# Optimization experiments

Measured on AMD Instinct MI355X. Metric: run time of the kernel, lower is better.

## Reference

```python
import jax, jax.numpy as jnp
import numpy as np

WS = 7  # window_size (odd)


def _attn_idx(H, W, ws):
    # replication-pad the arange over the valid (unfolded) grid, matching ReplicationPad2d
    Ho, Wo = H - (ws - 1), W - (ws - 1)
    idx = np.arange(Ho * Wo, dtype=np.int64).reshape(Ho, Wo)
    pad = ws // 2
    idx = np.pad(idx, pad, mode='edge')  # [H, W]
    return jnp.asarray(idx.reshape(-1))  # [H*W]


def _bias_idx(H, W, ws):
    rep_h = np.ones(ws, dtype=np.int64); rep_h[ws // 2] = H - (ws - 1)
    rep_w = np.ones(ws, dtype=np.int64); rep_w[ws // 2] = W - (ws - 1)
    idx_h = np.repeat(np.arange(ws), rep_h)  # [H]
    idx_w = np.repeat(np.arange(ws), rep_w)  # [W]
    bias_hw = idx_h[:, None] * (2 * ws - 1) + idx_w[None, :]  # [H, W]
    idx_k = (np.arange(ws)[:, None] * (2 * ws - 1) + np.arange(ws)).reshape(-1)  # [ws^2]
    bias_idx = bias_hw.reshape(-1)[:, None] + idx_k[None, :]  # [H*W, ws^2]
    return jnp.asarray(bias_idx)


def setup_inputs() -> dict:
    key = jax.random.key(0)
    k0, k1, k2, k3 = jax.random.split(key, 4)
    B, C, H, W = 2, 256, 56, 56
    nh = 8
    x = jax.random.normal(k0, (B, C, H, W), jnp.float32)
    qkv_w = jax.random.normal(k1, (3 * C, C), jnp.float32) * 0.02  # 1x1 conv weight
    qkv_b = jnp.zeros((3 * C,), jnp.float32)
    proj_w = jax.random.normal(k2, (C, C), jnp.float32) * 0.02  # 1x1 conv weight
    proj_b = jnp.zeros((C,), jnp.float32)
    relative_bias = jax.random.normal(k3, ((2 * WS - 1) ** 2, nh), jnp.float32) * 0.02
    return {"x": x, "qkv_w": qkv_w, "qkv_b": qkv_b,
            "proj_w": proj_w, "proj_b": proj_b, "relative_bias": relative_bias}


def reference(x, qkv_w, qkv_b, proj_w, proj_b, relative_bias):
    B, C, H, W = x.shape
    ws = WS
    nh = relative_bias.shape[1]
    hd = C // nh
    scale = hd ** -0.5
    L = (H - ws + 1) * (W - ws + 1)

    # 1x1 conv qkv
    qkv = jnp.einsum('oc,bchw->bohw', qkv_w, x) + qkv_b[None, :, None, None]
    q, k, v = qkv[:, :C], qkv[:, C:2 * C], qkv[:, 2 * C:]
    q = q * scale

    def unfold(t):
        # torch nn.Unfold: [B, C*ws^2, L] with channel-major ordering (c slowest),
        # then .view(B, C, -1, ws^2): row-major reinterpretation (faithful to source)
        p = jax.lax.conv_general_dilated_patches(t, (ws, ws), (1, 1), 'VALID')  # [B,C*ws^2,Ho,Wo]
        return p.reshape(B, C, L, ws * ws)

    attn_idx = _attn_idx(H, W, ws)   # [H*W] indices into L
    bias_idx = _bias_idx(H, W, ws)   # [H*W, ws^2]

    k_u = unfold(k).reshape(B, nh, hd, L, ws * ws).transpose(0, 1, 3, 2, 4)  # [B,nh,L,hd,ws^2]
    v_u = unfold(v).reshape(B, nh, hd, L, ws * ws).transpose(0, 1, 3, 4, 2)  # [B,nh,L,ws^2,hd]
    k_g = k_u[:, :, attn_idx]  # [B,nh,HW,hd,ws^2]
    v_g = v_u[:, :, attn_idx]  # [B,nh,HW,ws^2,hd]

    qh = q.reshape(B, nh, hd, H * W).transpose(0, 1, 3, 2)  # [B,nh,HW,hd]

    attn = jnp.einsum('bnld,bnldk->bnlk', qh, k_g)  # [B,nh,HW,ws^2]
    bias = jnp.transpose(relative_bias[bias_idx], (2, 0, 1))  # [nh,HW,ws^2]
    attn = attn + bias[None]  # NOTE: source applies no softmax; dropout p=0

    out = jnp.einsum('bnlk,bnlkd->bnld', attn, v_g)  # [B,nh,HW,hd]
    out = jnp.transpose(out, (0, 1, 3, 2)).reshape(B, C, H, W)
    out = jnp.einsum('oc,bchw->bohw', proj_w, out) + proj_b[None, :, None, None]
    return out
```

## Files before the change

kernel.cpp:

```cpp
#include <hip/hip_runtime.h>
#include <cstddef>
#include <cstdint>

#define HWT   3136
#define WIMG  56
#define CCH   256
#define NH    8
#define QKV_ELEMS (16 * HWT * 32)
#define SCALE 0.17677669529663687f

typedef __attribute__((ext_vector_type(8))) short short8;
typedef __attribute__((ext_vector_type(4))) short short4v;
typedef __attribute__((ext_vector_type(4))) float f32x4;
typedef _Float16 half2v __attribute__((ext_vector_type(2)));
typedef _Float16 half4v __attribute__((ext_vector_type(4)));
typedef _Float16 half8v __attribute__((ext_vector_type(8)));

#if defined(__has_builtin)
#if __has_builtin(__builtin_amdgcn_fdot2)
#define HAVE_FDOT2 1
#endif
#endif
#ifndef HAVE_FDOT2
#define HAVE_FDOT2 0
#endif

__device__ __forceinline__ ushort f2bf(float f) {
  union { float f; uint32_t u; } v; v.f = f;
  uint32_t u = v.u;
  u += 0x7fffu + ((u >> 16) & 1u);
  return (ushort)(u >> 16);
}

__global__ __launch_bounds__(256) void prep_k(
    const float* __restrict__ x, const float* __restrict__ qkv_w,
    const float* __restrict__ proj_w, ushort* __restrict__ xt,
    ushort* __restrict__ wq, ushort* __restrict__ wp,
    ushort* __restrict__ src16) {
  if (blockIdx.z == 3) {
    int e = (blockIdx.y * 98 + blockIdx.x) * 256 + threadIdx.x;
    if (e < 2500 * 49) {
      int sp = e / 2500;
      int pos = e - sp * 2500;
      int i = pos / 50 + sp / 7;
      int j = pos % 50 + sp % 7;
      src16[e] = (ushort)(i * WIMG + j);
    }
    return;
  }
  if (blockIdx.z == 2) {
    int base = ((blockIdx.y * 98 + blockIdx.x) * 256 + threadIdx.x) * 2;
#pragma unroll
    for (int e = base; e < base + 2; ++e) {
      if (e < 768 * 256) wq[e] = f2bf(qkv_w[e]);
      else if (e < 768 * 256 + 256 * 256) {
        int e2 = e - 768 * 256;
        wp[e2] = f2bf(proj_w[e2]);
      }
    }
    return;
  }
  __shared__ float tile[32][33];
  const int hw0 = blockIdx.x * 32, c0 = blockIdx.y * 32, b = blockIdx.z;
  const int tx = threadIdx.x & 31, ty = threadIdx.x >> 5;
  const float* xb = x + ((size_t)b * CCH + c0) * HWT + hw0;
#pragma unroll
  for (int i = 0; i < 4; ++i) {
    int c = ty + i * 8;
    tile[c][tx] = xb[(size_t)c * HWT + tx];
  }
  __syncthreads();
  ushort* xo = xt + ((size_t)b * HWT + hw0) * CCH + c0;
#pragma unroll
  for (int i = 0; i < 4; ++i) {
    int hwl = ty + i * 8;
    xo[(size_t)hwl * CCH + tx] = f2bf(tile[tx][hwl]);
  }
}

template <int MODE, int MI>
__global__ __launch_bounds__(256) void mfma_gemm_k(
    const ushort* __restrict__ A, int rowsA,
    const ushort* __restrict__ B, int rowsB,
    const float* __restrict__ biasv, void* __restrict__ outp) {
  __shared__ ushort Alds[MI * 32 * 32];
  __shared__ ushort Blds[64 * 32];

  const int t  = threadIdx.x;
  const int m0 = blockIdx.y * (MI * 32);
  const int n0 = blockIdx.x * 64;
  const int b  = blockIdx.z;

  const ushort* Ab = A;
  const ushort* Bb = B + (size_t)b * HWT * CCH;

  const int lane  = t & 63;
  const int wid   = t >> 6;
  const int wm    = (wid >> 1) * (MI * 16);
  const int wn    = (wid & 1) * 32;
  const int lrow  = lane & 15;
  const int cwant = lane >> 4;
  const int csw   = (cwant ^ ((lrow >> 1) & 3)) * 8;

  const int srow   = t >> 2;
  const int scslot = t & 3;
  const int wlds   = wid << 9;

  f32x4 acc[MI][2];
#pragma unroll
  for (int i = 0; i < MI; ++i)
#pragma unroll
    for (int j = 0; j < 2; ++j) acc[i][j] = (f32x4){0.f, 0.f, 0.f, 0.f};

  for (int k0 = 0; k0 < CCH; k0 += 32) {
    __syncthreads();
#pragma unroll
    for (int h = 0; h < (MI + 1) / 2; ++h) {
      const int lr = srow + h * 64;
      if (lr < MI * 32) {
        const int csrc = (scslot ^ ((lr >> 1) & 3)) * 8;
        int ga = m0 + lr; ga = ga < rowsA ? ga : rowsA - 1;
        const ushort* gpa = Ab + (size_t)ga * CCH + k0 + csrc;
        ushort* lpa = Alds + h * 2048 + wlds;
        __builtin_amdgcn_global_load_lds(
            (const __attribute__((address_space(1))) void*)gpa,
            (__attribute__((address_space(3))) void*)lpa, 16, 0, 0);
      }
    }
    {
      const int lr = srow;
      const int csrc = (scslot ^ ((lr >> 1) & 3)) * 8;
      int gb = n0 + lr; gb = gb < rowsB ? gb : rowsB - 1;
      const ushort* gpb = Bb + (size_t)gb * CCH + k0 + csrc;
      ushort* lpb = Blds + wlds;
      __builtin_amdgcn_global_load_lds(
          (const __attribute__((address_space(1))) void*)gpb,
          (__attribute__((address_space(3))) void*)lpb, 16, 0, 0);
    }
    __syncthreads();

    short8 af[MI], bf[2];
#pragma unroll
    for (int mi = 0; mi < MI; ++mi)
      af[mi] = *(const short8*)&Alds[(wm + mi * 16 + lrow) * 32 + csw];
#pragma unroll
    for (int ni = 0; ni < 2; ++ni)
      bf[ni] = *(const short8*)&Blds[(wn + ni * 16 + lrow) * 32 + csw];
#pragma unroll
    for (int mi = 0; mi < MI; ++mi)
#pragma unroll
      for (int ni = 0; ni < 2; ++ni)
        acc[mi][ni] = __builtin_amdgcn_mfma_f32_16x16x32_bf16(
            af[mi], bf[ni], acc[mi][ni], 0, 0, 0);
  }

  const int row4 = (lane >> 4) * 4;
  if (MODE == 0) {
    _Float16* qh = (_Float16*)outp;
#pragma unroll
    for (int mi = 0; mi < MI; ++mi) {
      const int o0 = m0 + wm + mi * 16 + row4;
      const int t3 = o0 >> 8, c0 = o0 & 255;
      const int head = c0 >> 5, d0 = c0 & 31;
      const float sc = (t3 == 0) ? SCALE : 1.f;
      float bv[4];
#pragma unroll
      for (int r = 0; r < 4; ++r) bv[r] = biasv[o0 + r];
      if (t3 == 1) {
        _Float16* base = qh + (size_t)QKV_ELEMS +
                         ((size_t)(b * NH + head) * 4 + (d0 >> 3)) * (HWT * 8) +
                         (d0 & 7);
#pragma unroll
        for (int ni = 0; ni < 2; ++ni) {
          const int hw = n0 + wn + ni * 16 + lrow;
          if (hw < HWT) {
            half4v pack;
#pragma unroll
            for (int r = 0; r < 4; ++r)
              pack[r] = (_Float16)(acc[mi][ni][r] + bv[r]);
            *(half4v*)(base + (size_t)hw * 8) = pack;
          }
        }
      } else {
        _Float16* base = qh + (size_t)t3 * QKV_ELEMS +
                         (size_t)(b * NH + head) * HWT * 32 + d0;
#pragma unroll
        for (int ni = 0; ni < 2; ++ni) {
          const int hw = n0 + wn + ni * 16 + lrow;
          if (hw < HWT) {
            half4v pack;
#pragma unroll
            for (int r = 0; r < 4; ++r)
              pack[r] = (_Float16)((acc[mi][ni][r] + bv[r]) * sc);
            *(half4v*)(base + (size_t)hw * 32) = pack;
          }
        }
      }
    }
  } else {
    float* op = (float*)outp;
#pragma unroll
    for (int mi = 0; mi < MI; ++mi)
#pragma unroll
      for (int r = 0; r < 4; ++r) {
        const int o = m0 + wm + mi * 16 + row4 + r;
        const float bvv = biasv[o];
#pragma unroll
        for (int ni = 0; ni < 2; ++ni) {
          const int hw = n0 + wn + ni * 16 + lrow;
          if (hw < HWT)
            op[((size_t)b * CCH + o) * HWT + hw] = acc[mi][ni][r] + bvv;
        }
      }
  }
}

__global__ __launch_bounds__(128, 5) void attn_v6_k(
    const _Float16* __restrict__ q_h, const _Float16* __restrict__ kt8,
    const _Float16* __restrict__ v_h, const float* __restrict__ relbias,
    const ushort* __restrict__ src16, ushort* __restrict__ att_t) {
  const int id  = blockIdx.x;
  const int idx = (id & 7) * 392 + (id >> 3);
  const int bn  = idx / 196;
  const int g   = idx % 196;
  const int px0 = g * 16;
  const int b = bn >> 3, n = bn & 7;

  __shared__ float bias_s[169];
  __shared__ uint32_t as_lds[16 * 49];
  __shared__ float part_lds[64][8];

  const int tid = threadIdx.x;
  for (int i = tid; i < 169; i += 128) bias_s[i] = relbias[i * NH + n];
  __syncthreads();

  const int wid = tid >> 6, lane = tid & 63;
  const int jc = lane < 49 ? lane : 48;
  const int jbias = (jc / 7) * 13 + jc % 7;

  const _Float16* kb = kt8 + (size_t)bn * 4 * HWT * 8;
  const _Float16* vb = v_h + (size_t)bn * HWT * 32;
  const _Float16* qb = q_h + (size_t)bn * HWT * 32;

  const int pxw = px0 + wid * 8;

  int sv[8], bb[8];
#pragma unroll
  for (int p = 0; p < 8; ++p) {
    const int px = pxw + p;
    const int h = px / WIMG, w = px % WIMG;
    int ph = h - 3; ph = ph < 0 ? 0 : (ph > 49 ? 49 : ph);
    int pw = w - 3; pw = pw < 0 ? 0 : (pw > 49 ? 49 : pw);
    const int l = ph * 50 + pw;
    const int bih = (h < 3) ? h : ((h < 53) ? 3 : h - 49);
    const int biw = (w < 3) ? w : ((w < 53) ? 3 : w - 49);
    bb[p] = bih * 13 + biw + jbias;
    sv[p] = (int)src16[l * 49 + jc];
  }

#pragma unroll
  for (int batch = 0; batch < 4; ++batch) {
    union V16 { uint4 u; half2v h2[4]; };
    V16 K[2][4];
#pragma unroll
    for (int p = 0; p < 2; ++p)
#pragma unroll
      for (int dq = 0; dq < 4; ++dq)
        K[p][dq].u =
            *(const uint4*)(kb + ((size_t)dq * HWT + sv[batch * 2 + p]) * 8);

#pragma unroll
    for (int p = 0; p < 2; ++p) {
      const int pp = batch * 2 + p;
      const int pxu = __builtin_amdgcn_readfirstlane(pxw + pp);
      union V64 { uint4 u[4]; half2v hv[16]; };
      V64 Q;
      const uint4* qp = (const uint4*)(qb + (size_t)pxu * 32);
#pragma unroll
      for (int i = 0; i < 4; ++i) Q.u[i] = qp[i];
      const float bvv = bias_s[bb[pp]];

      float a0 = 0.f, a1 = 0.f, a2 = 0.f, a3 = 0.f;
#if HAVE_FDOT2
#pragma unroll
      for (int i = 0; i < 4; ++i) {
        a0 = __builtin_amdgcn_fdot2(K[p][0].h2[i], Q.hv[i],      a0, false);
        a1 = __builtin_amdgcn_fdot2(K[p][1].h2[i], Q.hv[4 + i],  a1, false);
        a2 = __builtin_amdgcn_fdot2(K[p][2].h2[i], Q.hv[8 + i],  a2, false);
        a3 = __builtin_amdgcn_fdot2(K[p][3].h2[i], Q.hv[12 + i], a3, false);
      }
#else
#pragma unroll
      for (int i = 0; i < 4; ++i) {
        a0 += (float)K[p][0].h2[i][0] * (float)Q.hv[i][0] +
              (float)K[p][0].h2[i][1] * (float)Q.hv[i][1];
        a1 += (float)K[p][1].h2[i][0] * (float)Q.hv[4 + i][0] +
              (float)K[p][1].h2[i][1] * (float)Q.hv[4 + i][1];
        a2 += (float)K[p][2].h2[i][0] * (float)Q.hv[8 + i][0] +
              (float)K[p][2].h2[i][1] * (float)Q.hv[8 + i][1];
        a3 += (float)K[p][3].h2[i][0] * (float)Q.hv[12 + i][0] +
              (float)K[p][3].h2[i][1] * (float)Q.hv[12 + i][1];
      }
#endif
      const float a = (a0 + a1) + (a2 + a3) + bvv;
      union { _Float16 hh; uint16_t us; } cv;
      cv.hh = (_Float16)a;
      if (lane < 49)
        as_lds[(wid * 8 + pp) * 49 + lane] = ((uint32_t)sv[pp] << 16) | cv.us;
    }
  }
  __syncthreads();

  const int pxb = lane >> 2, oc4 = lane & 3;
  const _Float16* vbase = vb + oc4 * 8;
  const uint32_t* arow = &as_lds[pxb * 49];
  const int jbase = wid * 25;
  const int jcnt  = wid ? 24 : 25;

  float acc[8];
#pragma unroll
  for (int c = 0; c < 8; ++c) acc[c] = 0.f;

#pragma unroll
  for (int jj = 0; jj < 25; ++jj) {
    if (jj < jcnt) {
      const uint32_t u = arow[jbase + jj];
      union { uint16_t us; _Float16 hh; } cv;
      cv.us = (uint16_t)(u & 0xffffu);
      const float a = (float)cv.hh;
      const int s = (int)(u >> 16);
      const half8v vv = *(const half8v*)(vbase + (size_t)s * 32);
#pragma unroll
      for (int c = 0; c < 8; ++c) acc[c] += a * (float)vv[c];
    }
  }

  if (wid == 1) {
#pragma unroll
    for (int c = 0; c < 8; ++c) part_lds[lane][c] = acc[c];
  }
  __syncthreads();
  if (wid == 0) {
#pragma unroll
    for (int c = 0; c < 8; ++c) acc[c] += part_lds[lane][c];
    ushort tmp[8];
#pragma unroll
    for (int c = 0; c < 8; ++c) tmp[c] = f2bf(acc[c]);
    *(short8*)(att_t + ((size_t)b * HWT + px0 + pxb) * CCH + n * 32 + oc4 * 8) =
        *(const short8*)tmp;
  }
}

extern "C" void kernel_launch(void* const* d_in, const int* in_sizes, int n_in,
                              void* d_out, int out_size, void* d_ws, size_t ws_size,
                              hipStream_t stream) {
  const float* x       = (const float*)d_in[0];
  const float* qkv_w   = (const float*)d_in[1];
  const float* qkv_b   = (const float*)d_in[2];
  const float* proj_w  = (const float*)d_in[3];
  const float* proj_b  = (const float*)d_in[4];
  const float* relbias = (const float*)d_in[5];
  float* out = (float*)d_out;

  char* wsb = (char*)d_ws;
  _Float16* qh  = (_Float16*)wsb;
  _Float16* kt8 = qh + (size_t)QKV_ELEMS;
  _Float16* vh  = qh + (size_t)2 * QKV_ELEMS;
  ushort*   xt  = (ushort*)(wsb + (size_t)3 * QKV_ELEMS * 2);
  ushort*   wq  = xt + (size_t)QKV_ELEMS;
  ushort*   wp  = wq + 768 * 256;
  ushort*   src16 = wp + 256 * 256;
  ushort*   att_t = xt;

  hipLaunchKernelGGL(prep_k, dim3(98, 8, 4), dim3(256), 0, stream,
                     x, qkv_w, proj_w, xt, wq, wp, src16);
  hipLaunchKernelGGL((mfma_gemm_k<0, 2>), dim3(49, 12, 2), dim3(256), 0, stream,
                     wq, 768, xt, HWT, qkv_b, (void*)qh);
  hipLaunchKernelGGL(attn_v6_k, dim3(3136), dim3(128), 0, stream,
                     qh, kt8, vh, relbias, src16, att_t);
  hipLaunchKernelGGL((mfma_gemm_k<1, 1>), dim3(49, 8, 2), dim3(256), 0, stream,
                     wp, 256, att_t, HWT, proj_b, (void*)out);
}
```

Before: 49.45 us.

## Make attention warps independent: per-warp LDS rows, drop block syncs and reduction

The attention kernel's AV stage is restructured so each wavefront only consumes the scores it wrote to its own LDS region. This removes the mid-kernel __syncthreads and the cross-warp partial-sum reduction through LDS. Each lane now covers 4 channels over all 49 window positions instead of 8 channels over half of them. The source index and bias index are also packed into one register array, and launch bounds rise to 6 blocks per CU, to cut register and LDS pressure. The cost is a longer serial loop per lane and narrower V loads.

```diff
diff --git a/kernel.cpp b/kernel.cpp
--- a/kernel.cpp
+++ b/kernel.cpp
@@ -215,7 +215,7 @@
   }
 }
 
-__global__ __launch_bounds__(128, 5) void attn_v6_k(
+__global__ __launch_bounds__(128, 6) void attn_v7_k(
     const _Float16* __restrict__ q_h, const _Float16* __restrict__ kt8,
     const _Float16* __restrict__ v_h, const float* __restrict__ relbias,
     const ushort* __restrict__ src16, ushort* __restrict__ att_t) {
@@ -228,7 +228,6 @@
 
   __shared__ float bias_s[169];
   __shared__ uint32_t as_lds[16 * 49];
-  __shared__ float part_lds[64][8];
 
   const int tid = threadIdx.x;
   for (int i = tid; i < 169; i += 128) bias_s[i] = relbias[i * NH + n];
@@ -243,8 +242,9 @@
   const _Float16* qb = q_h + (size_t)bn * HWT * 32;
 
   const int pxw = px0 + wid * 8;
-
-  int sv[8], bb[8];
+  uint32_t* my_lds = &as_lds[wid * 8 * 49];
+
+  uint32_t pk[8];
 #pragma unroll
   for (int p = 0; p < 8; ++p) {
     const int px = pxw + p;
@@ -254,8 +254,8 @@
     const int l = ph * 50 + pw;
     const int bih = (h < 3) ? h : ((h < 53) ? 3 : h - 49);
     const int biw = (w < 3) ? w : ((w < 53) ? 3 : w - 49);
-    bb[p] = bih * 13 + biw + jbias;
-    sv[p] = (int)src16[l * 49 + jc];
+    pk[p] = ((uint32_t)src16[l * 49 + jc] << 8) |
+            (uint32_t)(bih * 13 + biw + jbias);
   }
 
 #pragma unroll
@@ -266,8 +266,8 @@
     for (int p = 0; p < 2; ++p)
 #pragma unroll
       for (int dq = 0; dq < 4; ++dq)
-        K[p][dq].u =
-            *(const uint4*)(kb + ((size_t)dq * HWT + sv[batch * 2 + p]) * 8);
+        K[p][dq].u = *(const uint4*)(
+            kb + ((size_t)dq * HWT + (pk[batch * 2 + p] >> 8)) * 8);
 
 #pragma unroll
     for (int p = 0; p < 2; ++p) {
@@ -278,7 +278,7 @@
       const uint4* qp = (const uint4*)(qb + (size_t)pxu * 32);
 #pragma unroll
       for (int i = 0; i < 4; ++i) Q.u[i] = qp[i];
-      const float bvv = bias_s[bb[pp]];
+      const float bvv = bias_s[pk[pp] & 0xffu];
 
       float a0 = 0.f, a1 = 0.f, a2 = 0.f, a3 = 0.f;
 #if HAVE_FDOT2
@@ -306,49 +306,34 @@
       union { _Float16 hh; uint16_t us; } cv;
       cv.hh = (_Float16)a;
       if (lane < 49)
-        as_lds[(wid * 8 + pp) * 49 + lane] = ((uint32_t)sv[pp] << 16) | cv.us;
-    }
-  }
-  __syncthreads();
-
-  const int pxb = lane >> 2, oc4 = lane & 3;
-  const _Float16* vbase = vb + oc4 * 8;
-  const uint32_t* arow = &as_lds[pxb * 49];
-  const int jbase = wid * 25;
-  const int jcnt  = wid ? 24 : 25;
-
-  float acc[8];
-#pragma unroll
-  for (int c = 0; c < 8; ++c) acc[c] = 0.f;
-
-#pragma unroll
-  for (int jj = 0; jj < 25; ++jj) {
-    if (jj < jcnt) {
-      const uint32_t u = arow[jbase + jj];
-      union { uint16_t us; _Float16 hh; } cv;
-      cv.us = (uint16_t)(u & 0xffffu);
-      const float a = (float)cv.hh;
-      const int s = (int)(u >> 16);
-      const half8v vv = *(const half8v*)(vbase + (size_t)s * 32);
-#pragma unroll
-      for (int c = 0; c < 8; ++c) acc[c] += a * (float)vv[c];
-    }
-  }
-
-  if (wid == 1) {
-#pragma unroll
-    for (int c = 0; c < 8; ++c) part_lds[lane][c] = acc[c];
-  }
-  __syncthreads();
-  if (wid == 0) {
-#pragma unroll
-    for (int c = 0; c < 8; ++c) acc[c] += part_lds[lane][c];
-    ushort tmp[8];
-#pragma unroll
-    for (int c = 0; c < 8; ++c) tmp[c] = f2bf(acc[c]);
-    *(short8*)(att_t + ((size_t)b * HWT + px0 + pxb) * CCH + n * 32 + oc4 * 8) =
-        *(const short8*)tmp;
-  }
+        my_lds[pp * 49 + lane] = ((pk[pp] >> 8) << 16) | cv.us;
+    }
+  }
+
+  const int pxb = lane >> 3, oc = lane & 7;
+  const uint32_t* arow = &my_lds[pxb * 49];
+  const _Float16* vbase = vb + oc * 4;
+
+  float c0 = 0.f, c1 = 0.f, c2 = 0.f, c3 = 0.f;
+#pragma unroll 7
+  for (int j = 0; j < 49; ++j) {
+    const uint32_t u = arow[j];
+    union { uint16_t us; _Float16 hh; } cv;
+    cv.us = (uint16_t)(u & 0xffffu);
+    const float a = (float)cv.hh;
+    const int s = (int)(u >> 16);
+    const half4v vv = *(const half4v*)(vbase + (size_t)s * 32);
+    c0 += a * (float)vv[0];
+    c1 += a * (float)vv[1];
+    c2 += a * (float)vv[2];
+    c3 += a * (float)vv[3];
+  }
+
+  ushort tmp[4];
+  tmp[0] = f2bf(c0); tmp[1] = f2bf(c1);
+  tmp[2] = f2bf(c2); tmp[3] = f2bf(c3);
+  *(short4v*)(att_t + ((size_t)b * HWT + pxw + pxb) * CCH + n * 32 + oc * 4) =
+      *(const short4v*)tmp;
 }
 
 extern "C" void kernel_launch(void* const* d_in, const int* in_sizes, int n_in,
@@ -376,7 +361,7 @@
                      x, qkv_w, proj_w, xt, wq, wp, src16);
   hipLaunchKernelGGL((mfma_gemm_k<0, 2>), dim3(49, 12, 2), dim3(256), 0, stream,
                      wq, 768, xt, HWT, qkv_b, (void*)qh);
-  hipLaunchKernelGGL(attn_v6_k, dim3(3136), dim3(128), 0, stream,
+  hipLaunchKernelGGL(attn_v7_k, dim3(3136), dim3(128), 0, stream,
                      qh, kt8, vh, relbias, src16, att_t);
   hipLaunchKernelGGL((mfma_gemm_k<1, 1>), dim3(49, 8, 2), dim3(256), 0, stream,
                      wp, 256, att_t, HWT, proj_b, (void*)out);
```

Result: slower. 50.57 us (+2.3%).

## Fuse fp32-to-bf16 conversion and transpose into QKV and projection GEMM loads

Applied to the files above, without the earlier changes.

Removes the separate prep kernel that transposed x to bf16 and converted the weights. The QKV GEMM now reads fp32 x and qkv_w directly, converts them in registers and stores them into padded LDS. The src16 index table is built by an extra row of blocks in the same launch. The projection GEMM converts proj_w on the fly. This saves one launch and a round trip through the intermediate buffers, but replaces async global_load_lds with strided scalar fp32 loads of x (8 rows per thread) and repeats the conversion work in every block.

```diff
diff --git a/kernel.cpp b/kernel.cpp
--- a/kernel.cpp
+++ b/kernel.cpp
@@ -8,6 +8,7 @@
 #define NH    8
 #define QKV_ELEMS (16 * HWT * 32)
 #define SCALE 0.17677669529663687f
+#define PAD   40
 
 typedef __attribute__((ext_vector_type(8))) short short8;
 typedef __attribute__((ext_vector_type(4))) short short4v;
@@ -32,106 +33,168 @@
   return (ushort)(u >> 16);
 }
 
-__global__ __launch_bounds__(256) void prep_k(
+__global__ __launch_bounds__(256) void gemm_qkv_k(
     const float* __restrict__ x, const float* __restrict__ qkv_w,
-    const float* __restrict__ proj_w, ushort* __restrict__ xt,
-    ushort* __restrict__ wq, ushort* __restrict__ wp,
+    const float* __restrict__ qkv_b, _Float16* __restrict__ qh,
     ushort* __restrict__ src16) {
-  if (blockIdx.z == 3) {
-    int e = (blockIdx.y * 98 + blockIdx.x) * 256 + threadIdx.x;
-    if (e < 2500 * 49) {
-      int sp = e / 2500;
-      int pos = e - sp * 2500;
-      int i = pos / 50 + sp / 7;
-      int j = pos % 50 + sp % 7;
-      src16[e] = (ushort)(i * WIMG + j);
+  if (blockIdx.y == 12) {
+    if (blockIdx.z == 0) {
+      for (int e = blockIdx.x * 256 + threadIdx.x; e < 2500 * 49;
+           e += 49 * 256) {
+        int sp = e / 2500;
+        int pos = e - sp * 2500;
+        int si = pos / 50;
+        int sj = pos - si * 50;
+        src16[e] = (ushort)((si + sp / 7) * WIMG + sj + sp % 7);
+      }
     }
     return;
   }
-  if (blockIdx.z == 2) {
-    int base = ((blockIdx.y * 98 + blockIdx.x) * 256 + threadIdx.x) * 2;
-#pragma unroll
-    for (int e = base; e < base + 2; ++e) {
-      if (e < 768 * 256) wq[e] = f2bf(qkv_w[e]);
-      else if (e < 768 * 256 + 256 * 256) {
-        int e2 = e - 768 * 256;
-        wp[e2] = f2bf(proj_w[e2]);
-      }
-    }
-    return;
-  }
-  __shared__ float tile[32][33];
-  const int hw0 = blockIdx.x * 32, c0 = blockIdx.y * 32, b = blockIdx.z;
-  const int tx = threadIdx.x & 31, ty = threadIdx.x >> 5;
-  const float* xb = x + ((size_t)b * CCH + c0) * HWT + hw0;
-#pragma unroll
-  for (int i = 0; i < 4; ++i) {
-    int c = ty + i * 8;
-    tile[c][tx] = xb[(size_t)c * HWT + tx];
-  }
-  __syncthreads();
-  ushort* xo = xt + ((size_t)b * HWT + hw0) * CCH + c0;
-#pragma unroll
-  for (int i = 0; i < 4; ++i) {
-    int hwl = ty + i * 8;
-    xo[(size_t)hwl * CCH + tx] = f2bf(tile[tx][hwl]);
-  }
-}
-
-template <int MODE, int MI>
-__global__ __launch_bounds__(256) void mfma_gemm_k(
-    const ushort* __restrict__ A, int rowsA,
-    const ushort* __restrict__ B, int rowsB,
-    const float* __restrict__ biasv, void* __restrict__ outp) {
-  __shared__ ushort Alds[MI * 32 * 32];
-  __shared__ ushort Blds[64 * 32];
+
+  __shared__ ushort Alds[64 * PAD];
+  __shared__ ushort Blds[64 * PAD];
 
   const int t  = threadIdx.x;
-  const int m0 = blockIdx.y * (MI * 32);
+  const int m0 = blockIdx.y * 64;
   const int n0 = blockIdx.x * 64;
   const int b  = blockIdx.z;
 
-  const ushort* Ab = A;
-  const ushort* Bb = B + (size_t)b * HWT * CCH;
-
-  const int lane  = t & 63;
-  const int wid   = t >> 6;
-  const int wm    = (wid >> 1) * (MI * 16);
-  const int wn    = (wid & 1) * 32;
-  const int lrow  = lane & 15;
+  const float* xb = x + (size_t)b * CCH * HWT;
+
+  const int lane = t & 63, wid = t >> 6;
+  const int wm = (wid >> 1) * 32, wn = (wid & 1) * 32;
+  const int lrow = lane & 15;
+  const int cw8  = (lane >> 4) * 8;
+
+  const int srow = t >> 2;
+  const int scs  = t & 3;
+
+  f32x4 acc[2][2];
+#pragma unroll
+  for (int i = 0; i < 2; ++i)
+#pragma unroll
+    for (int j = 0; j < 2; ++j) acc[i][j] = (f32x4){0.f, 0.f, 0.f, 0.f};
+
+  for (int k0 = 0; k0 < CCH; k0 += 32) {
+    __syncthreads();
+    {
+      const float* ap = qkv_w + (size_t)(m0 + srow) * CCH + k0 + scs * 8;
+      const float4 v0 = *(const float4*)ap;
+      const float4 v1 = *(const float4*)(ap + 4);
+      ushort tmp[8];
+      tmp[0] = f2bf(v0.x); tmp[1] = f2bf(v0.y);
+      tmp[2] = f2bf(v0.z); tmp[3] = f2bf(v0.w);
+      tmp[4] = f2bf(v1.x); tmp[5] = f2bf(v1.y);
+      tmp[6] = f2bf(v1.z); tmp[7] = f2bf(v1.w);
+      *(short8*)&Alds[srow * PAD + scs * 8] = *(const short8*)tmp;
+    }
+    {
+      const float* bp = xb + (size_t)(k0 + scs * 8) * HWT + n0 + srow;
+      ushort tmp[8];
+#pragma unroll
+      for (int i = 0; i < 8; ++i) tmp[i] = f2bf(bp[(size_t)i * HWT]);
+      *(short8*)&Blds[srow * PAD + scs * 8] = *(const short8*)tmp;
+    }
+    __syncthreads();
+
+    short8 af[2], bf[2];
+#pragma unroll
+    for (int mi = 0; mi < 2; ++mi)
+      af[mi] = *(const short8*)&Alds[(wm + mi * 16 + lrow) * PAD + cw8];
+#pragma unroll
+    for (int ni = 0; ni < 2; ++ni)
+      bf[ni] = *(const short8*)&Blds[(wn + ni * 16 + lrow) * PAD + cw8];
+#pragma unroll
+    for (int mi = 0; mi < 2; ++mi)
+#pragma unroll
+      for (int ni = 0; ni < 2; ++ni)
+        acc[mi][ni] = __builtin_amdgcn_mfma_f32_16x16x32_bf16(
+            af[mi], bf[ni], acc[mi][ni], 0, 0, 0);
+  }
+
+  const int row4 = (lane >> 4) * 4;
+#pragma unroll
+  for (int mi = 0; mi < 2; ++mi) {
+    const int o0 = m0 + wm + mi * 16 + row4;
+    const int t3 = o0 >> 8, c0 = o0 & 255;
+    const int head = c0 >> 5, d0 = c0 & 31;
+    const float sc = (t3 == 0) ? SCALE : 1.f;
+    float bv[4];
+#pragma unroll
+    for (int r = 0; r < 4; ++r) bv[r] = qkv_b[o0 + r];
+    if (t3 == 1) {
+      _Float16* base = qh + (size_t)QKV_ELEMS +
+                       ((size_t)(b * NH + head) * 4 + (d0 >> 3)) * (HWT * 8) +
+                       (d0 & 7);
+#pragma unroll
+      for (int ni = 0; ni < 2; ++ni) {
+        const int hw = n0 + wn + ni * 16 + lrow;
+        half4v pack;
+#pragma unroll
+        for (int r = 0; r < 4; ++r)
+          pack[r] = (_Float16)(acc[mi][ni][r] + bv[r]);
+        *(half4v*)(base + (size_t)hw * 8) = pack;
+      }
+    } else {
+      _Float16* base = qh + (size_t)t3 * QKV_ELEMS +
+                       (size_t)(b * NH + head) * HWT * 32 + d0;
+#pragma unroll
+      for (int ni = 0; ni < 2; ++ni) {
+        const int hw = n0 + wn + ni * 16 + lrow;
+        half4v pack;
+#pragma unroll
+        for (int r = 0; r < 4; ++r)
+          pack[r] = (_Float16)((acc[mi][ni][r] + bv[r]) * sc);
+        *(half4v*)(base + (size_t)hw * 32) = pack;
+      }
+    }
+  }
+}
+
+__global__ __launch_bounds__(256) void gemm_proj_k(
+    const ushort* __restrict__ att_t, const float* __restrict__ proj_w,
+    const float* __restrict__ proj_b, float* __restrict__ outp) {
+  __shared__ ushort Alds[32 * PAD];
+  __shared__ ushort Blds[64 * 32];
+
+  const int t  = threadIdx.x;
+  const int m0 = blockIdx.y * 32;
+  const int n0 = blockIdx.x * 64;
+  const int b  = blockIdx.z;
+
+  const ushort* Bb = att_t + (size_t)b * HWT * CCH;
+
+  const int lane = t & 63, wid = t >> 6;
+  const int wm = (wid >> 1) * 16, wn = (wid & 1) * 32;
+  const int lrow = lane & 15;
   const int cwant = lane >> 4;
-  const int csw   = (cwant ^ ((lrow >> 1) & 3)) * 8;
+  const int cw8 = cwant * 8;
+  const int csw = (cwant ^ ((lrow >> 1) & 3)) * 8;
 
   const int srow   = t >> 2;
   const int scslot = t & 3;
   const int wlds   = wid << 9;
 
-  f32x4 acc[MI][2];
-#pragma unroll
-  for (int i = 0; i < MI; ++i)
-#pragma unroll
-    for (int j = 0; j < 2; ++j) acc[i][j] = (f32x4){0.f, 0.f, 0.f, 0.f};
+  const int alr = t >> 3;
+  const int ac4 = t & 7;
+
+  f32x4 acc[2];
+  acc[0] = (f32x4){0.f, 0.f, 0.f, 0.f};
+  acc[1] = (f32x4){0.f, 0.f, 0.f, 0.f};
 
   for (int k0 = 0; k0 < CCH; k0 += 32) {
     __syncthreads();
-#pragma unroll
-    for (int h = 0; h < (MI + 1) / 2; ++h) {
-      const int lr = srow + h * 64;
-      if (lr < MI * 32) {
-        const int csrc = (scslot ^ ((lr >> 1) & 3)) * 8;
-        int ga = m0 + lr; ga = ga < rowsA ? ga : rowsA - 1;
-        const ushort* gpa = Ab + (size_t)ga * CCH + k0 + csrc;
-        ushort* lpa = Alds + h * 2048 + wlds;
-        __builtin_amdgcn_global_load_lds(
-            (const __attribute__((address_space(1))) void*)gpa,
-            (__attribute__((address_space(3))) void*)lpa, 16, 0, 0);
-      }
-    }
     {
-      const int lr = srow;
-      const int csrc = (scslot ^ ((lr >> 1) & 3)) * 8;
-      int gb = n0 + lr; gb = gb < rowsB ? gb : rowsB - 1;
-      const ushort* gpb = Bb + (size_t)gb * CCH + k0 + csrc;
+      const float4 v0 =
+          *(const float4*)(proj_w + (size_t)(m0 + alr) * CCH + k0 + ac4 * 4);
+      ushort tmp[4];
+      tmp[0] = f2bf(v0.x); tmp[1] = f2bf(v0.y);
+      tmp[2] = f2bf(v0.z); tmp[3] = f2bf(v0.w);
+      *(short4v*)&Alds[alr * PAD + ac4 * 4] = *(const short4v*)tmp;
+    }
+    {
+      const int csrc = (scslot ^ ((srow >> 1) & 3)) * 8;
+      const ushort* gpb = Bb + (size_t)(n0 + srow) * CCH + k0 + csrc;
       ushort* lpb = Blds + wlds;
       __builtin_amdgcn_global_load_lds(
           (const __attribute__((address_space(1))) void*)gpb,
@@ -139,79 +202,27 @@
     }
     __syncthreads();
 
-    short8 af[MI], bf[2];
-#pragma unroll
-    for (int mi = 0; mi < MI; ++mi)
-      af[mi] = *(const short8*)&Alds[(wm + mi * 16 + lrow) * 32 + csw];
+    short8 af, bf[2];
+    af = *(const short8*)&Alds[(wm + lrow) * PAD + cw8];
 #pragma unroll
     for (int ni = 0; ni < 2; ++ni)
       bf[ni] = *(const short8*)&Blds[(wn + ni * 16 + lrow) * 32 + csw];
 #pragma unroll
-    for (int mi = 0; mi < MI; ++mi)
-#pragma unroll
-      for (int ni = 0; ni < 2; ++ni)
-        acc[mi][ni] = __builtin_amdgcn_mfma_f32_16x16x32_bf16(
-            af[mi], bf[ni], acc[mi][ni], 0, 0, 0);
+    for (int ni = 0; ni < 2; ++ni)
+      acc[ni] = __builtin_amdgcn_mfma_f32_16x16x32_bf16(af, bf[ni], acc[ni],
+                                                        0, 0, 0);
   }
 
   const int row4 = (lane >> 4) * 4;
-  if (MODE == 0) {
-    _Float16* qh = (_Float16*)outp;
-#pragma unroll
-    for (int mi = 0; mi < MI; ++mi) {
-      const int o0 = m0 + wm + mi * 16 + row4;
-      const int t3 = o0 >> 8, c0 = o0 & 255;
-      const int head = c0 >> 5, d0 = c0 & 31;
-      const float sc = (t3 == 0) ? SCALE : 1.f;
-      float bv[4];
-#pragma unroll
-      for (int r = 0; r < 4; ++r) bv[r] = biasv[o0 + r];
-      if (t3 == 1) {
-        _Float16* base = qh + (size_t)QKV_ELEMS +
-                         ((size_t)(b * NH + head) * 4 + (d0 >> 3)) * (HWT * 8) +
-                         (d0 & 7);
-#pragma unroll
-        for (int ni = 0; ni < 2; ++ni) {
-          const int hw = n0 + wn + ni * 16 + lrow;
-          if (hw < HWT) {
-            half4v pack;
-#pragma unroll
-            for (int r = 0; r < 4; ++r)
-              pack[r] = (_Float16)(acc[mi][ni][r] + bv[r]);
-            *(half4v*)(base + (size_t)hw * 8) = pack;
-          }
-        }
-      } else {
-        _Float16* base = qh + (size_t)t3 * QKV_ELEMS +
-                         (size_t)(b * NH + head) * HWT * 32 + d0;
-#pragma unroll
-        for (int ni = 0; ni < 2; ++ni) {
-          const int hw = n0 + wn + ni * 16 + lrow;
-          if (hw < HWT) {
-            half4v pack;
-#pragma unroll
-            for (int r = 0; r < 4; ++r)
-              pack[r] = (_Float16)((acc[mi][ni][r] + bv[r]) * sc);
-            *(half4v*)(base + (size_t)hw * 32) = pack;
-          }
-        }
-      }
-    }
-  } else {
-    float* op = (float*)outp;
-#pragma unroll
-    for (int mi = 0; mi < MI; ++mi)
-#pragma unroll
-      for (int r = 0; r < 4; ++r) {
-        const int o = m0 + wm + mi * 16 + row4 + r;
-        const float bvv = biasv[o];
-#pragma unroll
-        for (int ni = 0; ni < 2; ++ni) {
-          const int hw = n0 + wn + ni * 16 + lrow;
-          if (hw < HWT)
-            op[((size_t)b * CCH + o) * HWT + hw] = acc[mi][ni][r] + bvv;
-        }
-      }
+#pragma unroll
+  for (int r = 0; r < 4; ++r) {
+    const int o = m0 + wm + row4 + r;
+    const float bvv = proj_b[o];
+#pragma unroll
+    for (int ni = 0; ni < 2; ++ni) {
+      const int hw = n0 + wn + ni * 16 + lrow;
+      outp[((size_t)b * CCH + o) * HWT + hw] = acc[ni][r] + bvv;
+    }
   }
 }
 
@@ -363,21 +374,16 @@
   float* out = (float*)d_out;
 
   char* wsb = (char*)d_ws;
-  _Float16* qh  = (_Float16*)wsb;
-  _Float16* kt8 = qh + (size_t)QKV_ELEMS;
-  _Float16* vh  = qh + (size_t)2 * QKV_ELEMS;
-  ushort*   xt  = (ushort*)(wsb + (size_t)3 * QKV_ELEMS * 2);
-  ushort*   wq  = xt + (size_t)QKV_ELEMS;
-  ushort*   wp  = wq + 768 * 256;
-  ushort*   src16 = wp + 256 * 256;
-  ushort*   att_t = xt;
-
-  hipLaunchKernelGGL(prep_k, dim3(98, 8, 4), dim3(256), 0, stream,
-                     x, qkv_w, proj_w, xt, wq, wp, src16);
-  hipLaunchKernelGGL((mfma_gemm_k<0, 2>), dim3(49, 12, 2), dim3(256), 0, stream,
-                     wq, 768, xt, HWT, qkv_b, (void*)qh);
+  _Float16* qh    = (_Float16*)wsb;
+  _Float16* kt8   = qh + (size_t)QKV_ELEMS;
+  _Float16* vh    = qh + (size_t)2 * QKV_ELEMS;
+  ushort*   src16 = (ushort*)(wsb + (size_t)3 * QKV_ELEMS * 2);
+  ushort*   att_t = src16 + 122512;
+
+  hipLaunchKernelGGL(gemm_qkv_k, dim3(49, 13, 2), dim3(256), 0, stream,
+                     x, qkv_w, qkv_b, qh, src16);
   hipLaunchKernelGGL(attn_v6_k, dim3(3136), dim3(128), 0, stream,
                      qh, kt8, vh, relbias, src16, att_t);
-  hipLaunchKernelGGL((mfma_gemm_k<1, 1>), dim3(49, 8, 2), dim3(256), 0, stream,
-                     wp, 256, att_t, HWT, proj_b, (void*)out);
-}
+  hipLaunchKernelGGL(gemm_proj_k, dim3(49, 8, 2), dim3(256), 0, stream,
+                     att_t, proj_w, proj_b, out);
+}
```

After: 49.86 us. No clear change (+0.8%).
